# Kernel optimization log

Measured on AMD Instinct MI355X. Metric: run time of the kernel, lower is better.

Reference implementation:

```python
import jax, jax.numpy as jnp
import numpy as np

B, N, D, K = 8, 262144, 16, 256
M_MAX = 1024  # cap on condensation points per event for the pairwise repulsion block
ATTR_W, REP_W = 1.0, 1.0
BETA_POS_W, BETA_NEG_SIG_W, BETA_NEG_BG_W, MARGIN_W = 10.0, 3.0, 6.0, 10.0
THR, MARGIN = 0.5, 0.3
ALPHA, GAMMA = 0.75, 2.0


def setup_inputs() -> dict:
    key = jax.random.key(0)
    k1, k2, k3, k4 = jax.random.split(key, 4)
    beta = jax.random.normal(k1, (B, N, 1), jnp.float32)
    embed = jax.random.normal(k2, (B, N, D), jnp.float32)
    slice_id = jax.random.randint(k3, (B, N), -1, K)          # -1 == background
    is_cp = jax.random.uniform(k4, (B, N)) < 0.001            # sparse condensation points
    return {"beta": beta, "embed": embed, "slice_id": slice_id, "is_cp": is_cp}


def _per_event(beta, emb, sid, cp):
    # beta [N], emb [N,D], sid [N] int, cp [N] bool
    f32 = beta.dtype
    valid = sid >= 0
    cpv = cp & valid
    seg = jnp.where(valid, sid, K).astype(jnp.int32)          # slot K = invalid/background bucket

    p = jax.nn.sigmoid(beta)
    ce1 = jax.nn.softplus(-beta)   # BCE-with-logits, target = 1
    ce0 = jax.nn.softplus(beta)    # BCE-with-logits, target = 0

    # ---- pos_bce: size-weighted per-instance focal BCE over CP hits ----
    focal = ALPHA * (1.0 - p) ** GAMMA * ce1
    cpf = cp.astype(f32)
    sum_f = jax.ops.segment_sum(focal * cpf, seg, num_segments=K + 1)[:K]
    cnt_cp = jax.ops.segment_sum(cpf, seg, num_segments=K + 1)[:K]
    inst_size = jax.ops.segment_sum(jnp.ones_like(beta), seg, num_segments=K + 1)[:K]
    has_cp = cnt_cp > 0
    mean_f = sum_f / jnp.maximum(cnt_cp, 1.0)
    w = jnp.where(has_cp, inst_size, 0.0)
    pos_bce = jnp.sum(w * mean_f) / jnp.maximum(jnp.sum(w), 1.0)

    # ---- negative / background BCE and margin terms ----
    ncpf = (~cp).astype(f32)
    n_ncp = jnp.sum(ncpf)
    neg_bce = jnp.where(n_ncp > 0, jnp.sum(ce0 * ncpf) / jnp.maximum(n_ncp, 1.0), 0.0)
    n_cp = jnp.sum(cpf)
    pos_margin = jnp.sum(jax.nn.relu(THR + MARGIN - p) * cpf) / jnp.maximum(n_cp, 1.0)
    neg_margin = jnp.where(n_ncp > 0,
                           jnp.sum(jax.nn.relu(p - (THR - MARGIN)) * ncpf) / jnp.maximum(n_ncp, 1.0), 0.0)
    bgf = (sid == -1).astype(f32)
    n_bg = jnp.sum(bgf)
    bg_bce = jnp.where(n_bg > 0, jnp.sum(ce0 * bgf) / jnp.maximum(n_bg, 1.0), 0.0)

    beta_loss = (BETA_POS_W * pos_bce + BETA_NEG_SIG_W * neg_bce +
                 BETA_NEG_BG_W * bg_bce + MARGIN_W * (pos_margin + neg_margin))

    # ---- attraction: per-instance mean sq-dist to the FIRST CP hit of that instance ----
    idx = jnp.where(cp, jnp.arange(N), N)
    first_idx = jax.ops.segment_min(idx, seg, num_segments=K + 1)[:K]   # N if instance has no CP
    anchor_k = emb[jnp.clip(first_idx, 0, N - 1)]                       # [K,D]
    anchor = anchor_k[jnp.clip(sid, 0, K - 1)]                          # [N,D]
    d2 = jnp.sum((emb - anchor) ** 2, axis=-1)
    s_d2 = jax.ops.segment_sum(d2 * valid.astype(f32), seg, num_segments=K + 1)[:K]
    attraction = ATTR_W * jnp.sum(jnp.where(has_cp, s_d2 / jnp.maximum(inst_size, 1.0), 0.0))

    # ---- repulsion: mean exp(-||ci-cj||^2) over all CP x CP pairs (incl. diagonal) ----
    order = jnp.argsort(jnp.where(cpv, jnp.arange(N), N))[:M_MAX]
    selv = cpv[order].astype(f32)                                       # [M]
    cp_emb = emb[order]                                                 # [M,D]
    pd2 = jnp.sum((cp_emb[:, None, :] - cp_emb[None, :, :]) ** 2, axis=-1)
    Mv = jnp.sum(cpv.astype(f32))
    rep = jnp.sum(jnp.exp(-pd2) * (selv[:, None] * selv[None, :])) / jnp.maximum(Mv * Mv, 1.0)
    repulsion = jnp.where(Mv > 1, REP_W * rep, 0.0)

    loss = beta_loss + attraction + repulsion
    ok = (jnp.sum(valid) > 0) & (Mv > 0)
    return loss, ok


def reference(beta, embed, slice_id, is_cp):
    beta2 = beta[..., 0]  # squeeze(-1)
    loss_b, ok_b = jax.vmap(_per_event)(beta2, embed, slice_id, is_cp)
    cnt = jnp.sum(ok_b.astype(beta2.dtype))
    total = jnp.sum(jnp.where(ok_b, loss_b, 0.0))
    return jnp.where(cnt > 0, total / jnp.maximum(cnt, 1.0), 0.0)
```

## Files before the change

kernel.cpp:

```cpp
#include <hip/hip_runtime.h>
#include <math.h>

#define Bn 8
#define Nn 262144
#define Kk 256
#define Dd 16
#define MCAP 4096
#define MSEL 1024
#define CHUNK 1024
#define NCH (Nn / CHUNK)
#define ASTR 17
#define CSTR 20

#define W_ATTR 1.0f
#define W_REP 1.0f
#define W_BPOS 10.0f
#define W_BNEG 3.0f
#define W_BBG 6.0f
#define W_MARG 10.0f
#define ALPHA_F 0.75f

#define OFF_SUMF 0
#define OFF_CNT 2048
#define OFF_SCAL 4096
#define OFF_MODE 4352
#define ZERO_WORDS 4356
#define OFF_FIRST 4356
#define OFF_CPIDX (OFF_FIRST + Bn*Kk)
#define OFF_PART (OFF_CPIDX + Bn*MCAP)
#define PART_WORDS ((size_t)Bn * NCH * Kk * 2)
#define WS_NEEDED (((size_t)OFF_PART + PART_WORDS) * 4)

__global__ void k_detect(const unsigned int* w, int* wsi) {
  const int stride = gridDim.x * blockDim.x;
  const int gid = blockIdx.x * blockDim.x + threadIdx.x;
  for (int i = gid; i < Bn * Kk; i += stride) wsi[OFF_FIRST + i] = 0x7FFFFFFF;
  int bad = 0;
  for (int i = gid; i < (Bn * Nn) / 4; i += stride) {
    unsigned int x = w[i];
    if (x > 1u && x != 0x3F800000u) bad = 1;
  }
  if (bad) atomicOr(&wsi[OFF_MODE], 1);
}

__global__ __launch_bounds__(256) void k_cplist(const float* __restrict__ beta,
                                                const int* __restrict__ sid,
                                                const void* __restrict__ cpp,
                                                float* wsf, int* wsi) {
  const int mode = wsi[OFF_MODE];
  const int stride = gridDim.x * blockDim.x;
  for (int i = blockIdx.x * blockDim.x + threadIdx.x; i < Bn * Nn; i += stride) {
    bool cp = mode ? (((const unsigned char*)cpp)[i] != 0)
                   : (((const unsigned int*)cpp)[i] != 0u);
    if (cp) {
      const int b = i >> 18;
      const int ii = i & (Nn - 1);
      const float x = beta[i];
      const float p = 1.f / (1.f + __expf(-x));
      const float sp = __logf(1.f + __expf(-fabsf(x)));
      const float ce0 = sp + fmaxf(x, 0.f);
      float* sc = wsf + OFF_SCAL + b * 32;
      atomicAdd(&sc[1], fmaxf(0.8f - p, 0.f));
      atomicAdd(&sc[4], 1.f);
      atomicAdd(&sc[11], ce0);
      atomicAdd(&sc[12], fmaxf(p - 0.2f, 0.f));
      const int s = sid[i];
      if (s >= 0) {
        const float ce1 = sp + fmaxf(-x, 0.f);
        const float om = 1.f - p;
        atomicAdd(&wsf[OFF_SUMF + b * Kk + s], ALPHA_F * om * om * ce1);
        atomicAdd(&wsi[OFF_CNT + b * Kk + s], 1);
        atomicMin(&wsi[OFF_FIRST + b * Kk + s], ii);
        int pos = atomicAdd(&wsi[OFF_SCAL + b * 32 + 6], 1);
        if (pos < MCAP) wsi[OFF_CPIDX + b * MCAP + pos] = ii;
      }
    }
  }
}

__global__ __launch_bounds__(256, 8) void k_pass(const float* __restrict__ beta,
                                                 const int* __restrict__ sid,
                                                 const float* __restrict__ embed,
                                                 float* wsf, int* wsi, int use_part) {
  const int b = blockIdx.y;
  const int ch = blockIdx.x;
  const int tid = threadIdx.x;
  __shared__ float ls_anch[Kk * ASTR];
  __shared__ float ls_d2[Kk];
  __shared__ int ls_inst[Kk];
  __shared__ float sred[4][4];
  {
    const int cnt = wsi[OFF_CNT + b * Kk + tid];
    const int fi = wsi[OFF_FIRST + b * Kk + tid];
    float* dst = &ls_anch[tid * ASTR];
    if (cnt > 0) {
      const float4* src = (const float4*)(embed + ((size_t)b * Nn + (size_t)fi) * Dd);
      float4 v0 = src[0], v1 = src[1], v2 = src[2], v3 = src[3];
      dst[0]=v0.x; dst[1]=v0.y; dst[2]=v0.z; dst[3]=v0.w;
      dst[4]=v1.x; dst[5]=v1.y; dst[6]=v1.z; dst[7]=v1.w;
      dst[8]=v2.x; dst[9]=v2.y; dst[10]=v2.z; dst[11]=v2.w;
      dst[12]=v3.x; dst[13]=v3.y; dst[14]=v3.z; dst[15]=v3.w;
    } else {
      #pragma unroll
      for (int d = 0; d < Dd; ++d) dst[d] = 0.f;
    }
  }
  ls_d2[tid] = 0.f;
  ls_inst[tid] = 0;
  __syncthreads();
  const int base = b * Nn;
  const float* eb = embed + (size_t)base * Dd;
  float a0 = 0.f, a2 = 0.f, a3 = 0.f, a5 = 0.f;
  {
    const int i0 = ch * CHUNK + tid * 4;
    int4 s4 = *(const int4*)(sid + base + i0);
    float4 b4 = *(const float4*)(beta + base + i0);
    float4 ev[16];
    #pragma unroll
    for (int q = 0; q < 16; ++q)
      ev[q] = *(const float4*)(eb + (size_t)(i0 + (q >> 2)) * Dd + (q & 3) * 4);
    const int ss[4] = {s4.x, s4.y, s4.z, s4.w};
    const float xs[4] = {b4.x, b4.y, b4.z, b4.w};
    #pragma unroll
    for (int j = 0; j < 4; ++j) {
      const int s = ss[j];
      const float x = xs[j];
      const float p = 1.f / (1.f + __expf(-x));
      const float sp = __logf(1.f + __expf(-fabsf(x)));
      const float ce0 = sp + fmaxf(x, 0.f);
      a0 += ce0;
      a2 += fmaxf(p - 0.2f, 0.f);
      if (s == -1) { a3 += ce0; a5 += 1.f; }
      const int scl = s >= 0 ? s : 0;
      const float* ar = &ls_anch[scl * ASTR];
      float4 v0 = ev[j * 4], v1 = ev[j * 4 + 1], v2 = ev[j * 4 + 2], v3 = ev[j * 4 + 3];
      float d2 = 0.f, df;
      df = v0.x - ar[0];  d2 += df * df;  df = v0.y - ar[1];  d2 += df * df;
      df = v0.z - ar[2];  d2 += df * df;  df = v0.w - ar[3];  d2 += df * df;
      df = v1.x - ar[4];  d2 += df * df;  df = v1.y - ar[5];  d2 += df * df;
      df = v1.z - ar[6];  d2 += df * df;  df = v1.w - ar[7];  d2 += df * df;
      df = v2.x - ar[8];  d2 += df * df;  df = v2.y - ar[9];  d2 += df * df;
      df = v2.z - ar[10]; d2 += df * df;  df = v2.w - ar[11]; d2 += df * df;
      df = v3.x - ar[12]; d2 += df * df;  df = v3.y - ar[13]; d2 += df * df;
      df = v3.z - ar[14]; d2 += df * df;  df = v3.w - ar[15]; d2 += df * df;
      if (s >= 0) {
        atomicAdd(&ls_inst[s], 1);
        atomicAdd(&ls_d2[s], d2);
      }
    }
  }
  __syncthreads();
  if (use_part) {
    float2* pb = (float2*)(wsf + OFF_PART + (((size_t)(b * NCH + ch)) * Kk + tid) * 2);
    *pb = make_float2(ls_d2[tid], (float)ls_inst[tid]);
  } else {
    atomicAdd(&wsf[OFF_SCAL + b * 32 + 10], 0.f);
  }
  for (int o = 32; o > 0; o >>= 1) {
    a0 += __shfl_down(a0, o); a2 += __shfl_down(a2, o);
    a3 += __shfl_down(a3, o); a5 += __shfl_down(a5, o);
  }
  const int wv = tid >> 6;
  if ((tid & 63) == 0) {
    sred[wv][0] = a0; sred[wv][1] = a2; sred[wv][2] = a3; sred[wv][3] = a5;
  }
  __syncthreads();
  if (tid == 0) {
    float s0 = 0, s2 = 0, s3 = 0, s5 = 0;
    for (int q = 0; q < 4; ++q) {
      s0 += sred[q][0]; s2 += sred[q][1]; s3 += sred[q][2]; s5 += sred[q][3];
    }
    atomicAdd(&wsf[OFF_SCAL + b * 32 + 0], s0);
    atomicAdd(&wsf[OFF_SCAL + b * 32 + 2], s2);
    atomicAdd(&wsf[OFF_SCAL + b * 32 + 3], s3);
    atomicAdd(&wsf[OFF_SCAL + b * 32 + 5], s5);
  }
}

__global__ __launch_bounds__(256) void k_redev(float* wsf, int* wsi) {
  const int b = blockIdx.x;
  const int t = threadIdx.x;
  const float2* p = (const float2*)(wsf + OFF_PART + (((size_t)b * NCH) * Kk + t) * 2);
  float d2s = 0.f, inst = 0.f;
  for (int ch = 0; ch < NCH; ++ch) {
    float2 v = p[(size_t)ch * Kk];
    d2s += v.x; inst += v.y;
  }
  const int cnt = wsi[OFF_CNT + b * Kk + t];
  const float sumf = wsf[OFF_SUMF + b * Kk + t];
  float attr_p = 0.f, w = 0.f, wf = 0.f;
  if (cnt > 0) {
    attr_p = d2s / fmaxf(inst, 1.f);
    w = inst;
    wf = inst * (sumf / fmaxf((float)cnt, 1.f));
  }
  for (int o = 32; o > 0; o >>= 1) {
    attr_p += __shfl_down(attr_p, o);
    w += __shfl_down(w, o);
    wf += __shfl_down(wf, o);
  }
  __shared__ float r3[3][4];
  if ((t & 63) == 0) { r3[0][t >> 6] = attr_p; r3[1][t >> 6] = w; r3[2][t >> 6] = wf; }
  __syncthreads();
  if (t == 0) {
    float at = r3[0][0] + r3[0][1] + r3[0][2] + r3[0][3];
    float sw = r3[1][0] + r3[1][1] + r3[1][2] + r3[1][3];
    float swf = r3[2][0] + r3[2][1] + r3[2][2] + r3[2][3];
    float pos_bce = swf / fmaxf(sw, 1.f);
    float* sc = wsf + OFF_SCAL + b * 32;
    const float ce0n = sc[0] - sc[11];
    const float rneg_s = sc[2] - sc[12];
    const float rpos = sc[1], ce0b = sc[3], ncp = sc[4], nbg = sc[5];
    const int mv = wsi[OFF_SCAL + b * 32 + 6];
    const float nncp = (float)Nn - ncp;
    const float neg_bce = nncp > 0.f ? ce0n / fmaxf(nncp, 1.f) : 0.f;
    const float pos_m = rpos / fmaxf(ncp, 1.f);
    const float neg_m = nncp > 0.f ? rneg_s / fmaxf(nncp, 1.f) : 0.f;
    const float bg_bce = nbg > 0.f ? ce0b / fmaxf(nbg, 1.f) : 0.f;
    sc[8] = W_BPOS * pos_bce + W_BNEG * neg_bce + W_BBG * bg_bce + W_MARG * (pos_m + neg_m);
    sc[10] = at;
    const float nvalid = (float)Nn - nbg;
    wsi[OFF_SCAL + b * 32 + 7] = (nvalid > 0.f && mv > 0) ? 1 : 0;
  }
}

__global__ __launch_bounds__(256) void k_rep(const float* __restrict__ embed,
                                             float* wsf, int* wsi) {
  const int b = blockIdx.y;
  const int t = threadIdx.x;
  __shared__ int sidx[MCAP];
  __shared__ float cemb[256 * CSTR];
  __shared__ float csq[256];
  __shared__ float red[4];
  const int mv = wsi[OFF_SCAL + b * 32 + 6];
  const int msel = mv < MSEL ? mv : MSEL;
  const int mload = mv < MCAP ? mv : MCAP;
  for (int i = t; i < MCAP; i += 256)
    sidx[i] = (i < mload) ? wsi[OFF_CPIDX + b * MCAP + i] : 0x7FFFFFFF;
  __syncthreads();
  if (mv > MSEL) {
    for (int ksz = 2; ksz <= MCAP; ksz <<= 1) {
      for (int j = ksz >> 1; j > 0; j >>= 1) {
        for (int e = t; e < MCAP; e += 256) {
          int ixj = e ^ j;
          if (ixj > e) {
            bool up = ((e & ksz) == 0);
            int x = sidx[e], y = sidx[ixj];
            if ((x > y) == up) { sidx[e] = y; sidx[ixj] = x; }
          }
        }
        __syncthreads();
      }
    }
  }
  const float* eb = embed + (size_t)b * Nn * Dd;
  const int row = blockIdx.x * 64 + (t & 63);
  const int cg = t >> 6;
  const bool rok = row < msel;
  float r[Dd];
  float rsq = 0.f;
  if (rok) {
    const float4* s = (const float4*)(eb + (size_t)sidx[row] * Dd);
    float4 v0 = s[0], v1 = s[1], v2 = s[2], v3 = s[3];
    r[0]=v0.x; r[1]=v0.y; r[2]=v0.z; r[3]=v0.w;
    r[4]=v1.x; r[5]=v1.y; r[6]=v1.z; r[7]=v1.w;
    r[8]=v2.x; r[9]=v2.y; r[10]=v2.z; r[11]=v2.w;
    r[12]=v3.x; r[13]=v3.y; r[14]=v3.z; r[15]=v3.w;
    #pragma unroll
    for (int d = 0; d < Dd; ++d) rsq += r[d] * r[d];
  }
  float acc = 0.f;
  for (int c0 = 0; c0 < msel; c0 += 256) {
    const int nc = (msel - c0) < 256 ? (msel - c0) : 256;
    __syncthreads();
    for (int wvi = t; wvi < nc * 4; wvi += 256) {
      int col = wvi >> 2, q = wvi & 3;
      float4 v = ((const float4*)(eb + (size_t)sidx[c0 + col] * Dd))[q];
      *(float4*)&cemb[col * CSTR + q * 4] = v;
    }
    __syncthreads();
    for (int col = t; col < nc; col += 256) {
      float s = 0.f;
      #pragma unroll
      for (int d = 0; d < Dd; ++d) s += cemb[col * CSTR + d] * cemb[col * CSTR + d];
      csq[col] = s;
    }
    __syncthreads();
    if (rok) {
      for (int c = cg; c < nc; c += 4) {
        float dotrc = 0.f;
        #pragma unroll
        for (int d = 0; d < Dd; ++d) dotrc += r[d] * cemb[c * CSTR + d];
        acc += __expf(2.f * dotrc - rsq - csq[c]);
      }
    }
  }
  for (int o = 32; o > 0; o >>= 1) acc += __shfl_down(acc, o);
  if ((t & 63) == 0) red[t >> 6] = acc;
  __syncthreads();
  if (t == 0) {
    float s = red[0] + red[1] + red[2] + red[3];
    if (s != 0.f) atomicAdd(&wsf[OFF_SCAL + b * 32 + 9], s);
  }
}

__global__ void k_final(float* wsf, int* wsi, float* out, int out_size) {
  const int t = threadIdx.x;
  if (t == 0) {
    float total = 0.f;
    int cnt = 0;
    for (int b = 0; b < Bn; ++b) {
      float* sc = wsf + OFF_SCAL + b * 32;
      int* sci = wsi + OFF_SCAL + b * 32;
      int mv = sci[6];
      if (sci[7]) {
        float mvf = (float)mv;
        float rep = (mv > 1) ? W_REP * sc[9] / fmaxf(mvf * mvf, 1.f) : 0.f;
        total += sc[8] + W_ATTR * sc[10] + rep;
        cnt++;
      }
    }
    out[0] = (cnt > 0) ? total / (float)cnt : 0.f;
  }
  for (int i = 1 + t; i < out_size; i += 256) out[i] = 0.f;
}

extern "C" void kernel_launch(void* const* d_in, const int* in_sizes, int n_in,
                              void* d_out, int out_size, void* d_ws, size_t ws_size,
                              hipStream_t stream) {
  const float* beta = (const float*)d_in[0];
  const float* embed = (const float*)d_in[1];
  const int* sid = (const int*)d_in[2];
  const void* cp = d_in[3];
  float* out = (float*)d_out;
  float* wsf = (float*)d_ws;
  int* wsi = (int*)d_ws;
  const int use_part = ws_size >= WS_NEEDED ? 1 : 0;

  hipMemsetAsync(d_ws, 0, (size_t)ZERO_WORDS * 4, stream);
  k_detect<<<256, 256, 0, stream>>>((const unsigned int*)cp, wsi);
  k_cplist<<<2048, 256, 0, stream>>>(beta, sid, cp, wsf, wsi);
  dim3 gp(NCH, Bn);
  k_pass<<<gp, 256, 0, stream>>>(beta, sid, embed, wsf, wsi, use_part);
  k_redev<<<Bn, 256, 0, stream>>>(wsf, wsi);
  dim3 gr(MSEL / 64, Bn);
  k_rep<<<gr, 256, 0, stream>>>(embed, wsf, wsi);
  k_final<<<1, 256, 0, stream>>>(wsf, wsi, out, out_size);
}
```

Baseline: 318.5 us.

## Precompute transposed anchors once, double chunk size, vectorize detect scan

Adds a small kernel that gathers each instance's anchor embedding once per event into a transposed global buffer. k_pass blocks then copy it into shared memory with coalesced float4 loads instead of each doing a scattered 256-row gather. k_pass now walks two 1024-element sub-chunks per block, which halves the grid and the partial-buffer writes, and k_detect reads uint4 vectors. A real fallback accumulation path for a small workspace is also added. The transposed shared layout may raise bank conflicts on the data-dependent anchor reads, and the extra launch adds overhead.

```diff
diff --git a/kernel.cpp b/kernel.cpp
--- a/kernel.cpp
+++ b/kernel.cpp
@@ -7,9 +7,8 @@
 #define Dd 16
 #define MCAP 4096
 #define MSEL 1024
-#define CHUNK 1024
+#define CHUNK 2048
 #define NCH (Nn / CHUNK)
-#define ASTR 17
 #define CSTR 20
 
 #define W_ATTR 1.0f
@@ -22,23 +21,27 @@
 
 #define OFF_SUMF 0
 #define OFF_CNT 2048
-#define OFF_SCAL 4096
-#define OFF_MODE 4352
-#define ZERO_WORDS 4356
-#define OFF_FIRST 4356
-#define OFF_CPIDX (OFF_FIRST + Bn*Kk)
+#define OFF_D2F 4096
+#define OFF_INSTF 6144
+#define OFF_SCAL 8192
+#define OFF_MODE 8448
+#define ZERO_WORDS 8452
+#define OFF_FIRST 8464
+#define OFF_ANCH (OFF_FIRST + Bn*Kk)
+#define OFF_CPIDX (OFF_ANCH + Bn*Kk*Dd)
 #define OFF_PART (OFF_CPIDX + Bn*MCAP)
 #define PART_WORDS ((size_t)Bn * NCH * Kk * 2)
 #define WS_NEEDED (((size_t)OFF_PART + PART_WORDS) * 4)
 
-__global__ void k_detect(const unsigned int* w, int* wsi) {
+__global__ void k_detect(const uint4* w4, int* wsi) {
   const int stride = gridDim.x * blockDim.x;
   const int gid = blockIdx.x * blockDim.x + threadIdx.x;
   for (int i = gid; i < Bn * Kk; i += stride) wsi[OFF_FIRST + i] = 0x7FFFFFFF;
   int bad = 0;
-  for (int i = gid; i < (Bn * Nn) / 4; i += stride) {
-    unsigned int x = w[i];
-    if (x > 1u && x != 0x3F800000u) bad = 1;
+  for (int i = gid; i < (Bn * Nn) / 16; i += stride) {
+    uint4 u = w4[i];
+    if ((u.x > 1u && u.x != 0x3F800000u) || (u.y > 1u && u.y != 0x3F800000u) ||
+        (u.z > 1u && u.z != 0x3F800000u) || (u.w > 1u && u.w != 0x3F800000u)) bad = 1;
   }
   if (bad) atomicOr(&wsi[OFF_MODE], 1);
 }
@@ -78,6 +81,29 @@
   }
 }
 
+__global__ __launch_bounds__(256) void k_anchor(const float* __restrict__ embed,
+                                                float* wsf, int* wsi) {
+  const int b = blockIdx.x;
+  const int t = threadIdx.x;
+  const int cnt = wsi[OFF_CNT + b * Kk + t];
+  const int fi = wsi[OFF_FIRST + b * Kk + t];
+  float v[Dd];
+  if (cnt > 0) {
+    const float4* src = (const float4*)(embed + ((size_t)b * Nn + (size_t)fi) * Dd);
+    float4 v0 = src[0], v1 = src[1], v2 = src[2], v3 = src[3];
+    v[0]=v0.x; v[1]=v0.y; v[2]=v0.z; v[3]=v0.w;
+    v[4]=v1.x; v[5]=v1.y; v[6]=v1.z; v[7]=v1.w;
+    v[8]=v2.x; v[9]=v2.y; v[10]=v2.z; v[11]=v2.w;
+    v[12]=v3.x; v[13]=v3.y; v[14]=v3.z; v[15]=v3.w;
+  } else {
+    #pragma unroll
+    for (int d = 0; d < Dd; ++d) v[d] = 0.f;
+  }
+  float* dst = wsf + OFF_ANCH + (size_t)b * (Kk * Dd);
+  #pragma unroll
+  for (int d = 0; d < Dd; ++d) dst[d * Kk + t] = v[d];
+}
+
 __global__ __launch_bounds__(256, 8) void k_pass(const float* __restrict__ beta,
                                                  const int* __restrict__ sid,
                                                  const float* __restrict__ embed,
@@ -85,25 +111,15 @@
   const int b = blockIdx.y;
   const int ch = blockIdx.x;
   const int tid = threadIdx.x;
-  __shared__ float ls_anch[Kk * ASTR];
+  __shared__ float ls_anchT[Kk * Dd];
   __shared__ float ls_d2[Kk];
   __shared__ int ls_inst[Kk];
   __shared__ float sred[4][4];
   {
-    const int cnt = wsi[OFF_CNT + b * Kk + tid];
-    const int fi = wsi[OFF_FIRST + b * Kk + tid];
-    float* dst = &ls_anch[tid * ASTR];
-    if (cnt > 0) {
-      const float4* src = (const float4*)(embed + ((size_t)b * Nn + (size_t)fi) * Dd);
-      float4 v0 = src[0], v1 = src[1], v2 = src[2], v3 = src[3];
-      dst[0]=v0.x; dst[1]=v0.y; dst[2]=v0.z; dst[3]=v0.w;
-      dst[4]=v1.x; dst[5]=v1.y; dst[6]=v1.z; dst[7]=v1.w;
-      dst[8]=v2.x; dst[9]=v2.y; dst[10]=v2.z; dst[11]=v2.w;
-      dst[12]=v3.x; dst[13]=v3.y; dst[14]=v3.z; dst[15]=v3.w;
-    } else {
-      #pragma unroll
-      for (int d = 0; d < Dd; ++d) dst[d] = 0.f;
-    }
+    const float4* src = (const float4*)(wsf + OFF_ANCH + (size_t)b * (Kk * Dd));
+    float4* dst = (float4*)ls_anchT;
+    #pragma unroll
+    for (int q = 0; q < 4; ++q) dst[q * 256 + tid] = src[q * 256 + tid];
   }
   ls_d2[tid] = 0.f;
   ls_inst[tid] = 0;
@@ -111,8 +127,8 @@
   const int base = b * Nn;
   const float* eb = embed + (size_t)base * Dd;
   float a0 = 0.f, a2 = 0.f, a3 = 0.f, a5 = 0.f;
-  {
-    const int i0 = ch * CHUNK + tid * 4;
+  for (int it = 0; it < CHUNK / 1024; ++it) {
+    const int i0 = ch * CHUNK + it * 1024 + tid * 4;
     int4 s4 = *(const int4*)(sid + base + i0);
     float4 b4 = *(const float4*)(beta + base + i0);
     float4 ev[16];
@@ -132,17 +148,13 @@
       a2 += fmaxf(p - 0.2f, 0.f);
       if (s == -1) { a3 += ce0; a5 += 1.f; }
       const int scl = s >= 0 ? s : 0;
-      const float* ar = &ls_anch[scl * ASTR];
-      float4 v0 = ev[j * 4], v1 = ev[j * 4 + 1], v2 = ev[j * 4 + 2], v3 = ev[j * 4 + 3];
-      float d2 = 0.f, df;
-      df = v0.x - ar[0];  d2 += df * df;  df = v0.y - ar[1];  d2 += df * df;
-      df = v0.z - ar[2];  d2 += df * df;  df = v0.w - ar[3];  d2 += df * df;
-      df = v1.x - ar[4];  d2 += df * df;  df = v1.y - ar[5];  d2 += df * df;
-      df = v1.z - ar[6];  d2 += df * df;  df = v1.w - ar[7];  d2 += df * df;
-      df = v2.x - ar[8];  d2 += df * df;  df = v2.y - ar[9];  d2 += df * df;
-      df = v2.z - ar[10]; d2 += df * df;  df = v2.w - ar[11]; d2 += df * df;
-      df = v3.x - ar[12]; d2 += df * df;  df = v3.y - ar[13]; d2 += df * df;
-      df = v3.z - ar[14]; d2 += df * df;  df = v3.w - ar[15]; d2 += df * df;
+      const float* e = (const float*)&ev[j * 4];
+      float d2 = 0.f;
+      #pragma unroll
+      for (int d = 0; d < Dd; ++d) {
+        float df = e[d] - ls_anchT[d * Kk + scl];
+        d2 += df * df;
+      }
       if (s >= 0) {
         atomicAdd(&ls_inst[s], 1);
         atomicAdd(&ls_d2[s], d2);
@@ -154,7 +166,8 @@
     float2* pb = (float2*)(wsf + OFF_PART + (((size_t)(b * NCH + ch)) * Kk + tid) * 2);
     *pb = make_float2(ls_d2[tid], (float)ls_inst[tid]);
   } else {
-    atomicAdd(&wsf[OFF_SCAL + b * 32 + 10], 0.f);
+    atomicAdd(&wsf[OFF_D2F + b * Kk + tid], ls_d2[tid]);
+    atomicAdd(&wsi[OFF_INSTF + b * Kk + tid], ls_inst[tid]);
   }
   for (int o = 32; o > 0; o >>= 1) {
     a0 += __shfl_down(a0, o); a2 += __shfl_down(a2, o);
@@ -177,14 +190,20 @@
   }
 }
 
-__global__ __launch_bounds__(256) void k_redev(float* wsf, int* wsi) {
+__global__ __launch_bounds__(256) void k_redev(float* wsf, int* wsi, int use_part) {
   const int b = blockIdx.x;
   const int t = threadIdx.x;
-  const float2* p = (const float2*)(wsf + OFF_PART + (((size_t)b * NCH) * Kk + t) * 2);
-  float d2s = 0.f, inst = 0.f;
-  for (int ch = 0; ch < NCH; ++ch) {
-    float2 v = p[(size_t)ch * Kk];
-    d2s += v.x; inst += v.y;
+  float d2s, inst;
+  if (use_part) {
+    const float2* p = (const float2*)(wsf + OFF_PART + (((size_t)b * NCH) * Kk + t) * 2);
+    d2s = 0.f; inst = 0.f;
+    for (int ch = 0; ch < NCH; ++ch) {
+      float2 v = p[(size_t)ch * Kk];
+      d2s += v.x; inst += v.y;
+    }
+  } else {
+    d2s = wsf[OFF_D2F + b * Kk + t];
+    inst = (float)wsi[OFF_INSTF + b * Kk + t];
   }
   const int cnt = wsi[OFF_CNT + b * Kk + t];
   const float sumf = wsf[OFF_SUMF + b * Kk + t];
@@ -338,11 +357,12 @@
   const int use_part = ws_size >= WS_NEEDED ? 1 : 0;
 
   hipMemsetAsync(d_ws, 0, (size_t)ZERO_WORDS * 4, stream);
-  k_detect<<<256, 256, 0, stream>>>((const unsigned int*)cp, wsi);
+  k_detect<<<256, 256, 0, stream>>>((const uint4*)cp, wsi);
   k_cplist<<<2048, 256, 0, stream>>>(beta, sid, cp, wsf, wsi);
+  k_anchor<<<Bn, 256, 0, stream>>>(embed, wsf, wsi);
   dim3 gp(NCH, Bn);
   k_pass<<<gp, 256, 0, stream>>>(beta, sid, embed, wsf, wsi, use_part);
-  k_redev<<<Bn, 256, 0, stream>>>(wsf, wsi);
+  k_redev<<<Bn, 256, 0, stream>>>(wsf, wsi, use_part);
   dim3 gr(MSEL / 64, Bn);
   k_rep<<<gr, 256, 0, stream>>>(embed, wsf, wsi);
   k_final<<<1, 256, 0, stream>>>(wsf, wsi, out, out_size);
```

Result: faster. 293.5 us (-7.8%).
